# Kernel optimization log

Hardware: AMD Instinct MI355X
Metric: run time of the kernel (lower is better)

## Reference

```python
import jax, jax.numpy as jnp
import numpy as np

D = 128        # feature_dims
ITERS = 2      # update_iters
B, R = 8, 256  # n segments (proteins), residues per segment
NEG_SLOPE = 0.1

def leaky(x):
    return jax.nn.leaky_relu(x, NEG_SLOPE)

def setup_inputs() -> dict:
    key = jax.random.key(0)
    ks = jax.random.split(key, 13)
    def w(k, shape):
        fan_in = shape[0]
        return jax.random.normal(k, shape, jnp.float32) / np.sqrt(fan_in)
    return {
        "fresidues": jax.random.normal(ks[0], (B, R, 20), jnp.float32),
        "coordinates": jax.random.normal(ks[1], (B, R, 3), jnp.float32) * 10.0,
        "W_emb": w(ks[2], (20, D)),                    # res_embedding (no bias)
        "W_e1": w(ks[3], (2 * D + 1, D)),              # linear_e layer 1
        "b_e1": jnp.zeros((D,), jnp.float32),
        "W_e2": w(ks[4], (D, D)),                      # linear_e layer 2
        "b_e2": jnp.zeros((D,), jnp.float32),
        "W_inf": w(ks[5], (D, 1)),                     # linear_inf gate
        "b_inf": jnp.zeros((1,), jnp.float32),
        "W_h1": w(ks[6], (2 * D, D)),                  # linear_h layer 1
        "b_h1": jnp.zeros((D,), jnp.float32),
        "W_h2": w(ks[7], (D, D)),                      # linear_h layer 2
        "b_h2": jnp.zeros((D,), jnp.float32),
    }

def reference(fresidues, coordinates, W_emb, W_e1, b_e1, W_e2, b_e2,
              W_inf, b_inf, W_h1, b_h1, W_h2, b_h2):
    # h: [B,R,D]
    h = leaky(fresidues @ W_emb)
    # pairwise squared distances: [B,R,R,1], constant across iterations
    d2 = jnp.sum(jnp.square(coordinates[:, :, None, :] - coordinates[:, None, :, :]),
                 axis=-1, keepdims=True)
    # mask out self-edges (1 - eye): [1,R,R,1]
    mask = (1.0 - jnp.eye(R, dtype=h.dtype))[None, :, :, None]
    # split edge-MLP first-layer weights to avoid materializing the [B,R,R,2D+1] concat:
    # m_input = cat([h_i, h_j, d2]) @ W_e1  ==  h_i@W_i + h_j@W_j + d2*w_d
    W_i, W_j, w_d = W_e1[:D], W_e1[D:2 * D], W_e1[2 * D]
    for _ in range(ITERS):
        ti = h @ W_i                                   # [B,R,D] receiver part
        tj = h @ W_j                                   # [B,R,D] sender part
        pre = ti[:, :, None, :] + tj[:, None, :, :] + d2 * w_d + b_e1  # [B,R,R,D]
        m = leaky(leaky(pre) @ W_e2 + b_e2)            # [B,R,R,D]
        e = jax.nn.sigmoid(m @ W_inf + b_inf) * mask   # [B,R,R,1]
        m_pre = jnp.sum(m * e, axis=2)                 # sum over senders j -> [B,R,D]
        hm = jnp.concatenate([h, m_pre], axis=-1)      # [B,R,2D]
        h = (leaky(hm @ W_h1 + b_h1) @ W_h2 + b_h2) + h
    return h

if __name__ == "__main__":
    out = reference(**setup_inputs())
    print(out.shape, out.dtype)
```

## Files before the change

kernel.cpp:

```cpp
#include <hip/hip_runtime.h>

typedef unsigned short ushort_t;
typedef __attribute__((ext_vector_type(8))) short shortx8;
typedef __attribute__((ext_vector_type(4))) float floatx4;
typedef __attribute__((ext_vector_type(2))) float floatx2;

#define NS 0.1f

__device__ __forceinline__ ushort_t f2bf_rne(float f) {
  union { float f; unsigned int u; } v; v.f = f;
  unsigned int r = v.u + 0x7FFFu + ((v.u >> 16) & 1u);
  return (ushort_t)(r >> 16);
}
__device__ __forceinline__ unsigned int pk2bf(float a, float b) {
  union { float f; unsigned int u; } x, y; x.f = a; y.f = b;
  return __builtin_amdgcn_perm(y.u + 0x8000u, x.u + 0x8000u, 0x07060302u);
}
__device__ __forceinline__ ushort_t f2bf_rhu(float f) {
  union { float f; unsigned int u; } v; v.f = f;
  return (ushort_t)((v.u + 0x8000u) >> 16);
}
__device__ __forceinline__ float lk(float x) { return fmaxf(x, NS * x); }
__device__ __forceinline__ floatx2 lk2(floatx2 v) {
  return __builtin_elementwise_max(v, v * (floatx2){NS, NS});
}

__global__ __launch_bounds__(256) void prep_w(
    const float* __restrict__ W_e1, const float* __restrict__ W_e2,
    const float* __restrict__ W_h1, const float* __restrict__ W_h2,
    ushort_t* __restrict__ wijf, ushort_t* __restrict__ we2f,
    ushort_t* __restrict__ wh1f, ushort_t* __restrict__ wh2f) {
  int e = blockIdx.x * 256 + threadIdx.x;
  int which, le;
  if (e < 32768) { which = 0; le = e; }
  else if (e < 49152) { which = 1; le = e - 32768; }
  else if (e < 81920) { which = 2; le = e - 49152; }
  else { which = 3; le = e - 81920; }
  const int NT = (which == 0) ? 16 : 8;
  int f = le >> 3, j = le & 7;
  int lane = f & 63, ft = f >> 6;
  int t = ft % NT, s = ft / NT;
  int n = t * 16 + (lane & 15), k = s * 32 + (lane >> 4) * 8 + j;
  float v; ushort_t* d;
  if (which == 0) { v = (n < 128) ? W_e1[k * 128 + n] : W_e1[(128 + k) * 128 + (n - 128)]; d = wijf; }
  else if (which == 1) { v = W_e2[k * 128 + n]; d = we2f; }
  else if (which == 2) { v = W_h1[k * 128 + n]; d = wh1f; }
  else { v = W_h2[k * 128 + n]; d = wh2f; }
  d[le] = f2bf_rne(v);
}

__device__ __forceinline__ void proj_store(float v, int m, int n,
                                           float* __restrict__ ti, float* __restrict__ tjf) {
  if (n < 128) {
    ti[(size_t)m * 128 + n] = v;
  } else {
    int k = n - 128, b = m >> 8, j = m & 255;
    int s = k >> 5, lg2 = (k >> 3) & 3, j8 = k & 7;
    tjf[((((size_t)(b * 4 + s)) * 256 + j) * 4 + lg2) * 8 + j8] = v;
  }
}

__global__ __launch_bounds__(256) void h0_proj(
    const float* __restrict__ fres, const float* __restrict__ Wemb,
    const ushort_t* __restrict__ wijf, float* __restrict__ h_out,
    float* __restrict__ ti, float* __restrict__ tjf) {
  const int m0 = blockIdx.x * 16;
  const int tid = threadIdx.x;
  const int w = tid >> 6, lane = tid & 63, l16 = lane & 15, lg = lane >> 4;
  __shared__ __align__(16) ushort_t sH[16][136];
  {
    const int row = tid >> 4, c0 = (tid & 15) * 8;
    const float* fr = fres + (size_t)(m0 + row) * 20;
    float a[8] = {0, 0, 0, 0, 0, 0, 0, 0};
    for (int k = 0; k < 20; ++k) {
      float fv = fr[k];
      float4 w0 = *(const float4*)(Wemb + k * 128 + c0);
      float4 w1 = *(const float4*)(Wemb + k * 128 + c0 + 4);
      a[0] += fv * w0.x; a[1] += fv * w0.y; a[2] += fv * w0.z; a[3] += fv * w0.w;
      a[4] += fv * w1.x; a[5] += fv * w1.y; a[6] += fv * w1.z; a[7] += fv * w1.w;
    }
#pragma unroll
    for (int x = 0; x < 8; ++x) a[x] = lk(a[x]);
    float* ho = h_out + (size_t)(m0 + row) * 128 + c0;
    *(float4*)ho = (float4){a[0], a[1], a[2], a[3]};
    *(float4*)(ho + 4) = (float4){a[4], a[5], a[6], a[7]};
    unsigned int* sh = (unsigned int*)&sH[row][c0];
    sh[0] = pk2bf(a[0], a[1]); sh[1] = pk2bf(a[2], a[3]);
    sh[2] = pk2bf(a[4], a[5]); sh[3] = pk2bf(a[6], a[7]);
  }
  __syncthreads();
  floatx4 ap[4];
#pragma unroll
  for (int q = 0; q < 4; ++q) ap[q] = (floatx4){0.f, 0.f, 0.f, 0.f};
  const shortx8* Wp = (const shortx8*)wijf;
#pragma unroll
  for (int s = 0; s < 4; ++s) {
    shortx8 af = *(const shortx8*)&sH[l16][s * 32 + lg * 8];
#pragma unroll
    for (int q = 0; q < 4; ++q)
      ap[q] = __builtin_amdgcn_mfma_f32_16x16x32_bf16(af, Wp[(s * 16 + 4 * w + q) * 64 + lane], ap[q], 0, 0, 0);
  }
#pragma unroll
  for (int q = 0; q < 4; ++q) {
    const int n = (4 * w + q) * 16 + l16;
#pragma unroll
    for (int r = 0; r < 4; ++r) proj_store(ap[q][r], m0 + lg * 4 + r, n, ti, tjf);
  }
}

__global__ __launch_bounds__(256, 3) void edge_kernel(
    const float* __restrict__ ti, const float* __restrict__ tjf,
    const float* __restrict__ coords, const ushort_t* __restrict__ we2f,
    const float* __restrict__ W_e1, const float* __restrict__ b_e1,
    const float* __restrict__ b_e2, const float* __restrict__ W_inf,
    const float* __restrict__ b_inf, float* __restrict__ mp0, float* __restrict__ mp1) {
  const int blk = blockIdx.x;
  const int b = blk >> 9, i = (blk >> 1) & 255, ch = blk & 1;
  const int tid = threadIdx.x;
  const int w = tid >> 6, lane = tid & 63, l16 = lane & 15, lg = lane >> 4;

  __shared__ __align__(16) ushort_t sW[16384];
  __shared__ __align__(16) float sTiP[128];
  __shared__ __align__(16) float sWd[128];
  __shared__ __align__(16) float sD2[128];
  __shared__ __align__(16) float sMp[4][128];

  {
    shortx8* dst = (shortx8*)sW;
    const shortx8* src = (const shortx8*)we2f;
#pragma unroll
    for (int r = 0; r < 8; ++r) dst[r * 256 + tid] = src[r * 256 + tid];
  }
  if (tid < 128) {
    sTiP[tid] = ti[(size_t)(b * 256 + i) * 128 + tid] + b_e1[tid];
    sWd[tid] = W_e1[256 * 128 + tid];
    const int j = ch * 128 + tid;
    float dx = coords[(size_t)(b * 256 + i) * 3 + 0] - coords[(size_t)(b * 256 + j) * 3 + 0];
    float dy = coords[(size_t)(b * 256 + i) * 3 + 1] - coords[(size_t)(b * 256 + j) * 3 + 1];
    float dz = coords[(size_t)(b * 256 + i) * 3 + 2] - coords[(size_t)(b * 256 + j) * 3 + 2];
    sD2[tid] = dx * dx + dy * dy + dz * dz;
  }
  floatx4 acc[2][8];
#pragma unroll
  for (int t = 0; t < 8; ++t) {
    float bv = b_e2[t * 16 + l16];
    acc[0][t] = (floatx4){bv, bv, bv, bv};
    acc[1][t] = acc[0][t];
  }
  __syncthreads();

  float d2a[2];
  d2a[0] = sD2[w * 16 + l16];
  d2a[1] = sD2[64 + w * 16 + l16];
  const shortx8* sWf = (const shortx8*)sW;

#pragma unroll
  for (int s = 0; s < 4; ++s) {
    const int k0 = s * 32 + lg * 8;
    floatx2 p2[4], w2[4];
#pragma unroll
    for (int x = 0; x < 4; ++x) {
      p2[x] = *(const floatx2*)&sTiP[k0 + 2 * x];
      w2[x] = *(const floatx2*)&sWd[k0 + 2 * x];
    }
    shortx8 af[2];
#pragma unroll
    for (int c = 0; c < 2; ++c) {
      const int jr = ch * 128 + c * 64 + w * 16 + l16;
      const float* tb = tjf + (((size_t)(b * 4 + s) * 256 + jr) * 4 + lg) * 8;
      float4 t0 = *(const float4*)tb;
      float4 t1 = *(const float4*)(tb + 4);
      const floatx2 d2v = (floatx2){d2a[c], d2a[c]};
      floatx2 pr0 = (floatx2){t0.x, t0.y} + (p2[0] + d2v * w2[0]);
      floatx2 pr1 = (floatx2){t0.z, t0.w} + (p2[1] + d2v * w2[1]);
      floatx2 pr2 = (floatx2){t1.x, t1.y} + (p2[2] + d2v * w2[2]);
      floatx2 pr3 = (floatx2){t1.z, t1.w} + (p2[3] + d2v * w2[3]);
      floatx2 l0 = lk2(pr0), l1 = lk2(pr1), l2 = lk2(pr2), l3 = lk2(pr3);
      union { shortx8 s8; unsigned int u[4]; } A;
      A.u[0] = pk2bf(l0.x, l0.y); A.u[1] = pk2bf(l1.x, l1.y);
      A.u[2] = pk2bf(l2.x, l2.y); A.u[3] = pk2bf(l3.x, l3.y);
      af[c] = A.s8;
    }
#pragma unroll
    for (int tg = 0; tg < 2; ++tg) {
      shortx8 b0 = sWf[(s * 8 + tg * 4 + 0) * 64 + lane];
      shortx8 b1 = sWf[(s * 8 + tg * 4 + 1) * 64 + lane];
      shortx8 b2 = sWf[(s * 8 + tg * 4 + 2) * 64 + lane];
      shortx8 b3 = sWf[(s * 8 + tg * 4 + 3) * 64 + lane];
#pragma unroll
      for (int c = 0; c < 2; ++c) {
        acc[c][tg * 4 + 0] = __builtin_amdgcn_mfma_f32_16x16x32_bf16(af[c], b0, acc[c][tg * 4 + 0], 0, 0, 0);
        acc[c][tg * 4 + 1] = __builtin_amdgcn_mfma_f32_16x16x32_bf16(af[c], b1, acc[c][tg * 4 + 1], 0, 0, 0);
        acc[c][tg * 4 + 2] = __builtin_amdgcn_mfma_f32_16x16x32_bf16(af[c], b2, acc[c][tg * 4 + 2], 0, 0, 0);
        acc[c][tg * 4 + 3] = __builtin_amdgcn_mfma_f32_16x16x32_bf16(af[c], b3, acc[c][tg * 4 + 3], 0, 0, 0);
      }
    }
  }

  float winfv[8], mp[8];
#pragma unroll
  for (int t = 0; t < 8; ++t) { winfv[t] = W_inf[t * 16 + l16]; mp[t] = 0.f; }
  const float binf = b_inf[0];
#pragma unroll
  for (int c = 0; c < 2; ++c) {
#pragma unroll
    for (int t = 0; t < 8; ++t) {
      floatx2 v0 = lk2((floatx2){acc[c][t][0], acc[c][t][1]});
      floatx2 v1 = lk2((floatx2){acc[c][t][2], acc[c][t][3]});
      acc[c][t][0] = v0.x; acc[c][t][1] = v0.y; acc[c][t][2] = v1.x; acc[c][t][3] = v1.y;
    }
    float p[4];
#pragma unroll
    for (int r = 0; r < 4; ++r) {
      float sum = 0.f;
#pragma unroll
      for (int t = 0; t < 8; ++t) sum += acc[c][t][r] * winfv[t];
      p[r] = sum;
    }
#pragma unroll
    for (int off = 1; off <= 8; off <<= 1)
#pragma unroll
      for (int r = 0; r < 4; ++r) p[r] += __shfl_xor(p[r], off);
#pragma unroll
    for (int r = 0; r < 4; ++r) {
      const int jg = ch * 128 + c * 64 + w * 16 + lg * 4 + r;
      float x = p[r] + binf;
      float e = __builtin_amdgcn_rcpf(1.f + __expf(-x));
      if (jg == i) e = 0.f;
#pragma unroll
      for (int t = 0; t < 8; ++t) mp[t] += acc[c][t][r] * e;
    }
  }
#pragma unroll
  for (int t = 0; t < 8; ++t) {
    mp[t] += __shfl_xor(mp[t], 16);
    mp[t] += __shfl_xor(mp[t], 32);
  }
  if (lg == 0) {
#pragma unroll
    for (int t = 0; t < 8; ++t) sMp[w][t * 16 + l16] = mp[t];
  }
  __syncthreads();
  if (tid < 128) {
    float v = sMp[0][tid] + sMp[1][tid] + sMp[2][tid] + sMp[3][tid];
    float* mpo = ch ? mp1 : mp0;
    mpo[(size_t)(b * 256 + i) * 128 + tid] = v;
  }
}

__global__ __launch_bounds__(256) void node_kernel(
    const float* __restrict__ h_in, const float* __restrict__ mp0, const float* __restrict__ mp1,
    const ushort_t* __restrict__ wh1f, const float* __restrict__ b_h1,
    const ushort_t* __restrict__ wh2f, const float* __restrict__ b_h2,
    const ushort_t* __restrict__ wijf, float* __restrict__ h_out,
    float* __restrict__ ti, float* __restrict__ tjf, const int do_proj) {
  const int m0 = blockIdx.x * 16;
  const int tid = threadIdx.x;
  const int w = tid >> 6, lane = tid & 63, l16 = lane & 15, lg = lane >> 4;
  __shared__ __align__(16) ushort_t sA[16][264];
  __shared__ __align__(16) ushort_t sU[16][136];
  __shared__ __align__(16) ushort_t sHp[16][136];

  {
    const int row = tid >> 4, c0 = (tid & 15) * 16;
    unsigned int* dst = (unsigned int*)&sA[row][c0];
    if (c0 < 128) {
      const float* src = h_in + (size_t)(m0 + row) * 128 + c0;
#pragma unroll
      for (int x = 0; x < 8; ++x) dst[x] = pk2bf(src[2 * x], src[2 * x + 1]);
    } else {
      const float* s0 = mp0 + (size_t)(m0 + row) * 128 + (c0 - 128);
      const float* s1 = mp1 + (size_t)(m0 + row) * 128 + (c0 - 128);
#pragma unroll
      for (int x = 0; x < 8; ++x)
        dst[x] = pk2bf(s0[2 * x] + s1[2 * x], s0[2 * x + 1] + s1[2 * x + 1]);
    }
  }
  __syncthreads();
  floatx4 au[2];
#pragma unroll
  for (int q = 0; q < 2; ++q) { float bv = b_h1[(2 * w + q) * 16 + l16]; au[q] = (floatx4){bv, bv, bv, bv}; }
  const shortx8* W1 = (const shortx8*)wh1f;
#pragma unroll
  for (int s = 0; s < 8; ++s) {
    shortx8 af = *(const shortx8*)&sA[l16][s * 32 + lg * 8];
#pragma unroll
    for (int q = 0; q < 2; ++q)
      au[q] = __builtin_amdgcn_mfma_f32_16x16x32_bf16(af, W1[(s * 8 + 2 * w + q) * 64 + lane], au[q], 0, 0, 0);
  }
#pragma unroll
  for (int q = 0; q < 2; ++q)
#pragma unroll
    for (int r = 0; r < 4; ++r)
      sU[lg * 4 + r][(2 * w + q) * 16 + l16] = f2bf_rhu(lk(au[q][r]));
  __syncthreads();
  floatx4 ah[2];
#pragma unroll
  for (int q = 0; q < 2; ++q) { float bv = b_h2[(2 * w + q) * 16 + l16]; ah[q] = (floatx4){bv, bv, bv, bv}; }
  const shortx8* W2 = (const shortx8*)wh2f;
#pragma unroll
  for (int s = 0; s < 4; ++s) {
    shortx8 af = *(const shortx8*)&sU[l16][s * 32 + lg * 8];
#pragma unroll
    for (int q = 0; q < 2; ++q)
      ah[q] = __builtin_amdgcn_mfma_f32_16x16x32_bf16(af, W2[(s * 8 + 2 * w + q) * 64 + lane], ah[q], 0, 0, 0);
  }
#pragma unroll
  for (int q = 0; q < 2; ++q) {
    const int n = (2 * w + q) * 16 + l16;
#pragma unroll
    for (int r = 0; r < 4; ++r) {
      const int m = m0 + lg * 4 + r;
      float v = ah[q][r] + h_in[(size_t)m * 128 + n];
      h_out[(size_t)m * 128 + n] = v;
      sHp[lg * 4 + r][n] = f2bf_rhu(v);
    }
  }
  if (!do_proj) return;
  __syncthreads();
  floatx4 ap[4];
#pragma unroll
  for (int q = 0; q < 4; ++q) ap[q] = (floatx4){0.f, 0.f, 0.f, 0.f};
  const shortx8* Wp = (const shortx8*)wijf;
#pragma unroll
  for (int s = 0; s < 4; ++s) {
    shortx8 af = *(const shortx8*)&sHp[l16][s * 32 + lg * 8];
#pragma unroll
    for (int q = 0; q < 4; ++q)
      ap[q] = __builtin_amdgcn_mfma_f32_16x16x32_bf16(af, Wp[(s * 16 + 4 * w + q) * 64 + lane], ap[q], 0, 0, 0);
  }
#pragma unroll
  for (int q = 0; q < 4; ++q) {
    const int n = (4 * w + q) * 16 + l16;
#pragma unroll
    for (int r = 0; r < 4; ++r) proj_store(ap[q][r], m0 + lg * 4 + r, n, ti, tjf);
  }
}

extern "C" void kernel_launch(void* const* d_in, const int* in_sizes, int n_in,
                              void* d_out, int out_size, void* d_ws, size_t ws_size,
                              hipStream_t stream) {
  const float* fres   = (const float*)d_in[0];
  const float* coords = (const float*)d_in[1];
  const float* W_emb  = (const float*)d_in[2];
  const float* W_e1   = (const float*)d_in[3];
  const float* b_e1   = (const float*)d_in[4];
  const float* W_e2   = (const float*)d_in[5];
  const float* b_e2   = (const float*)d_in[6];
  const float* W_inf  = (const float*)d_in[7];
  const float* b_inf  = (const float*)d_in[8];
  const float* W_h1   = (const float*)d_in[9];
  const float* b_h1   = (const float*)d_in[10];
  const float* W_h2   = (const float*)d_in[11];
  const float* b_h2   = (const float*)d_in[12];
  float* out = (float*)d_out;

  char* ws = (char*)d_ws;
  float* hA  = (float*)(ws + (0 << 20));
  float* hB  = (float*)(ws + (1 << 20));
  float* tib = (float*)(ws + (2 << 20));
  float* tjf = (float*)(ws + (3 << 20));
  float* mp0 = (float*)(ws + (4 << 20));
  float* mp1 = (float*)(ws + (5 << 20));
  ushort_t* wijf = (ushort_t*)(ws + (6 << 20));
  ushort_t* we2f = wijf + 32768;
  ushort_t* wh1f = we2f + 16384;
  ushort_t* wh2f = wh1f + 32768;

  prep_w<<<384, 256, 0, stream>>>(W_e1, W_e2, W_h1, W_h2, wijf, we2f, wh1f, wh2f);
  h0_proj<<<128, 256, 0, stream>>>(fres, W_emb, wijf, hA, tib, tjf);

  edge_kernel<<<4096, 256, 0, stream>>>(tib, tjf, coords, we2f, W_e1, b_e1, b_e2, W_inf, b_inf, mp0, mp1);
  node_kernel<<<128, 256, 0, stream>>>(hA, mp0, mp1, wh1f, b_h1, wh2f, b_h2, wijf, hB, tib, tjf, 1);

  edge_kernel<<<4096, 256, 0, stream>>>(tib, tjf, coords, we2f, W_e1, b_e1, b_e2, W_inf, b_inf, mp0, mp1);
  node_kernel<<<128, 256, 0, stream>>>(hB, mp0, mp1, wh1f, b_h1, wh2f, b_h2, wijf, out, tib, tjf, 0);
}
```

Baseline: 180.2 us.

## Fuse all phases into one persistent cooperative kernel with grid syncs

Replaces the six separate kernel launches with one cooperative persistent kernel that runs the phases (weight prep, h0 projection, edge, node, edge, node) separated by grid-wide syncs. The edge phase now loops over several (segment, receiver, half) units per block and loads the W_e2 tile into shared memory once per block instead of once per unit. This removes launch gaps and repeated weight staging. In exchange it adds grid-sync overhead, caps the grid at 1024 blocks, and leaves most blocks idle during the small node phases. A fallback multi-launch path is kept.

```diff
diff --git a/kernel.cpp b/kernel.cpp
--- a/kernel.cpp
+++ b/kernel.cpp
@@ -1,4 +1,7 @@
 #include <hip/hip_runtime.h>
+#include <hip/hip_cooperative_groups.h>
+
+namespace cg = cooperative_groups;
 
 typedef unsigned short ushort_t;
 typedef __attribute__((ext_vector_type(8))) short shortx8;
@@ -25,354 +28,399 @@
   return __builtin_elementwise_max(v, v * (floatx2){NS, NS});
 }
 
-__global__ __launch_bounds__(256) void prep_w(
-    const float* __restrict__ W_e1, const float* __restrict__ W_e2,
-    const float* __restrict__ W_h1, const float* __restrict__ W_h2,
-    ushort_t* __restrict__ wijf, ushort_t* __restrict__ we2f,
-    ushort_t* __restrict__ wh1f, ushort_t* __restrict__ wh2f) {
-  int e = blockIdx.x * 256 + threadIdx.x;
-  int which, le;
-  if (e < 32768) { which = 0; le = e; }
-  else if (e < 49152) { which = 1; le = e - 32768; }
-  else if (e < 81920) { which = 2; le = e - 49152; }
-  else { which = 3; le = e - 81920; }
-  const int NT = (which == 0) ? 16 : 8;
-  int f = le >> 3, j = le & 7;
-  int lane = f & 63, ft = f >> 6;
-  int t = ft % NT, s = ft / NT;
-  int n = t * 16 + (lane & 15), k = s * 32 + (lane >> 4) * 8 + j;
-  float v; ushort_t* d;
-  if (which == 0) { v = (n < 128) ? W_e1[k * 128 + n] : W_e1[(128 + k) * 128 + (n - 128)]; d = wijf; }
-  else if (which == 1) { v = W_e2[k * 128 + n]; d = we2f; }
-  else if (which == 2) { v = W_h1[k * 128 + n]; d = wh1f; }
-  else { v = W_h2[k * 128 + n]; d = wh2f; }
-  d[le] = f2bf_rne(v);
-}
-
-__device__ __forceinline__ void proj_store(float v, int m, int n,
-                                           float* __restrict__ ti, float* __restrict__ tjf) {
+struct Prm {
+  const float* fres; const float* coords; const float* W_emb;
+  const float* W_e1; const float* b_e1; const float* W_e2; const float* b_e2;
+  const float* W_inf; const float* b_inf; const float* W_h1; const float* b_h1;
+  const float* W_h2; const float* b_h2;
+  float* out; float* hA; float* hB; float* tib; float* tjf; float* mp0; float* mp1;
+  ushort_t* wijf; ushort_t* we2f; ushort_t* wh1f; ushort_t* wh2f;
+};
+
+__device__ __forceinline__ void proj_store(const Prm& p, float v, int m, int n) {
   if (n < 128) {
-    ti[(size_t)m * 128 + n] = v;
+    p.tib[(size_t)m * 128 + n] = v;
   } else {
     int k = n - 128, b = m >> 8, j = m & 255;
     int s = k >> 5, lg2 = (k >> 3) & 3, j8 = k & 7;
-    tjf[((((size_t)(b * 4 + s)) * 256 + j) * 4 + lg2) * 8 + j8] = v;
-  }
-}
-
-__global__ __launch_bounds__(256) void h0_proj(
-    const float* __restrict__ fres, const float* __restrict__ Wemb,
-    const ushort_t* __restrict__ wijf, float* __restrict__ h_out,
-    float* __restrict__ ti, float* __restrict__ tjf) {
-  const int m0 = blockIdx.x * 16;
+    p.tjf[((((size_t)(b * 4 + s)) * 256 + j) * 4 + lg2) * 8 + j8] = v;
+  }
+}
+
+__device__ void phase_prep(const Prm& p) {
+  for (int e = blockIdx.x * 256 + threadIdx.x; e < 98304; e += gridDim.x * 256) {
+    int which, le;
+    if (e < 32768) { which = 0; le = e; }
+    else if (e < 49152) { which = 1; le = e - 32768; }
+    else if (e < 81920) { which = 2; le = e - 49152; }
+    else { which = 3; le = e - 81920; }
+    const int NT = (which == 0) ? 16 : 8;
+    int f = le >> 3, j = le & 7;
+    int lane = f & 63, ft = f >> 6;
+    int t = ft % NT, s = ft / NT;
+    int n = t * 16 + (lane & 15), k = s * 32 + (lane >> 4) * 8 + j;
+    float v; ushort_t* d;
+    if (which == 0) { v = (n < 128) ? p.W_e1[k * 128 + n] : p.W_e1[(128 + k) * 128 + (n - 128)]; d = p.wijf; }
+    else if (which == 1) { v = p.W_e2[k * 128 + n]; d = p.we2f; }
+    else if (which == 2) { v = p.W_h1[k * 128 + n]; d = p.wh1f; }
+    else { v = p.W_h2[k * 128 + n]; d = p.wh2f; }
+    d[le] = f2bf_rne(v);
+  }
+}
+
+__device__ void phase_h0proj(const Prm& p, char* smem) {
+  ushort_t (*sH)[136] = (ushort_t(*)[136])smem;
   const int tid = threadIdx.x;
   const int w = tid >> 6, lane = tid & 63, l16 = lane & 15, lg = lane >> 4;
-  __shared__ __align__(16) ushort_t sH[16][136];
-  {
-    const int row = tid >> 4, c0 = (tid & 15) * 8;
-    const float* fr = fres + (size_t)(m0 + row) * 20;
-    float a[8] = {0, 0, 0, 0, 0, 0, 0, 0};
-    for (int k = 0; k < 20; ++k) {
-      float fv = fr[k];
-      float4 w0 = *(const float4*)(Wemb + k * 128 + c0);
-      float4 w1 = *(const float4*)(Wemb + k * 128 + c0 + 4);
-      a[0] += fv * w0.x; a[1] += fv * w0.y; a[2] += fv * w0.z; a[3] += fv * w0.w;
-      a[4] += fv * w1.x; a[5] += fv * w1.y; a[6] += fv * w1.z; a[7] += fv * w1.w;
-    }
-#pragma unroll
-    for (int x = 0; x < 8; ++x) a[x] = lk(a[x]);
-    float* ho = h_out + (size_t)(m0 + row) * 128 + c0;
-    *(float4*)ho = (float4){a[0], a[1], a[2], a[3]};
-    *(float4*)(ho + 4) = (float4){a[4], a[5], a[6], a[7]};
-    unsigned int* sh = (unsigned int*)&sH[row][c0];
-    sh[0] = pk2bf(a[0], a[1]); sh[1] = pk2bf(a[2], a[3]);
-    sh[2] = pk2bf(a[4], a[5]); sh[3] = pk2bf(a[6], a[7]);
-  }
-  __syncthreads();
-  floatx4 ap[4];
-#pragma unroll
-  for (int q = 0; q < 4; ++q) ap[q] = (floatx4){0.f, 0.f, 0.f, 0.f};
-  const shortx8* Wp = (const shortx8*)wijf;
-#pragma unroll
-  for (int s = 0; s < 4; ++s) {
-    shortx8 af = *(const shortx8*)&sH[l16][s * 32 + lg * 8];
-#pragma unroll
-    for (int q = 0; q < 4; ++q)
-      ap[q] = __builtin_amdgcn_mfma_f32_16x16x32_bf16(af, Wp[(s * 16 + 4 * w + q) * 64 + lane], ap[q], 0, 0, 0);
-  }
-#pragma unroll
-  for (int q = 0; q < 4; ++q) {
-    const int n = (4 * w + q) * 16 + l16;
-#pragma unroll
-    for (int r = 0; r < 4; ++r) proj_store(ap[q][r], m0 + lg * 4 + r, n, ti, tjf);
-  }
-}
-
-__global__ __launch_bounds__(256, 3) void edge_kernel(
-    const float* __restrict__ ti, const float* __restrict__ tjf,
-    const float* __restrict__ coords, const ushort_t* __restrict__ we2f,
-    const float* __restrict__ W_e1, const float* __restrict__ b_e1,
-    const float* __restrict__ b_e2, const float* __restrict__ W_inf,
-    const float* __restrict__ b_inf, float* __restrict__ mp0, float* __restrict__ mp1) {
-  const int blk = blockIdx.x;
-  const int b = blk >> 9, i = (blk >> 1) & 255, ch = blk & 1;
+  for (int blk = blockIdx.x; blk < 128; blk += gridDim.x) {
+    const int m0 = blk * 16;
+    {
+      const int row = tid >> 4, c0 = (tid & 15) * 8;
+      const float* fr = p.fres + (size_t)(m0 + row) * 20;
+      float a[8] = {0, 0, 0, 0, 0, 0, 0, 0};
+      for (int k = 0; k < 20; ++k) {
+        float fv = fr[k];
+        float4 w0 = *(const float4*)(p.W_emb + k * 128 + c0);
+        float4 w1 = *(const float4*)(p.W_emb + k * 128 + c0 + 4);
+        a[0] += fv * w0.x; a[1] += fv * w0.y; a[2] += fv * w0.z; a[3] += fv * w0.w;
+        a[4] += fv * w1.x; a[5] += fv * w1.y; a[6] += fv * w1.z; a[7] += fv * w1.w;
+      }
+#pragma unroll
+      for (int x = 0; x < 8; ++x) a[x] = lk(a[x]);
+      float* ho = p.hA + (size_t)(m0 + row) * 128 + c0;
+      *(float4*)ho = (float4){a[0], a[1], a[2], a[3]};
+      *(float4*)(ho + 4) = (float4){a[4], a[5], a[6], a[7]};
+      unsigned int* sh = (unsigned int*)&sH[row][c0];
+      sh[0] = pk2bf(a[0], a[1]); sh[1] = pk2bf(a[2], a[3]);
+      sh[2] = pk2bf(a[4], a[5]); sh[3] = pk2bf(a[6], a[7]);
+    }
+    __syncthreads();
+    floatx4 ap[4];
+#pragma unroll
+    for (int q = 0; q < 4; ++q) ap[q] = (floatx4){0.f, 0.f, 0.f, 0.f};
+    const shortx8* Wp = (const shortx8*)p.wijf;
+#pragma unroll
+    for (int s = 0; s < 4; ++s) {
+      shortx8 af = *(const shortx8*)&sH[l16][s * 32 + lg * 8];
+#pragma unroll
+      for (int q = 0; q < 4; ++q)
+        ap[q] = __builtin_amdgcn_mfma_f32_16x16x32_bf16(af, Wp[(s * 16 + 4 * w + q) * 64 + lane], ap[q], 0, 0, 0);
+    }
+#pragma unroll
+    for (int q = 0; q < 4; ++q) {
+      const int n = (4 * w + q) * 16 + l16;
+#pragma unroll
+      for (int r = 0; r < 4; ++r) proj_store(p, ap[q][r], m0 + lg * 4 + r, n);
+    }
+    __syncthreads();
+  }
+}
+
+__device__ void phase_edge(const Prm& p, char* smem) {
   const int tid = threadIdx.x;
   const int w = tid >> 6, lane = tid & 63, l16 = lane & 15, lg = lane >> 4;
-
-  __shared__ __align__(16) ushort_t sW[16384];
-  __shared__ __align__(16) float sTiP[128];
-  __shared__ __align__(16) float sWd[128];
-  __shared__ __align__(16) float sD2[128];
-  __shared__ __align__(16) float sMp[4][128];
-
+  ushort_t* sW = (ushort_t*)smem;
+  float* sTiP = (float*)(smem + 32768);
+  float* sWd  = (float*)(smem + 33280);
+  float* sD2  = (float*)(smem + 33792);
+  float* sMp  = (float*)(smem + 34304);
   {
     shortx8* dst = (shortx8*)sW;
-    const shortx8* src = (const shortx8*)we2f;
+    const shortx8* src = (const shortx8*)p.we2f;
 #pragma unroll
     for (int r = 0; r < 8; ++r) dst[r * 256 + tid] = src[r * 256 + tid];
-  }
-  if (tid < 128) {
-    sTiP[tid] = ti[(size_t)(b * 256 + i) * 128 + tid] + b_e1[tid];
-    sWd[tid] = W_e1[256 * 128 + tid];
-    const int j = ch * 128 + tid;
-    float dx = coords[(size_t)(b * 256 + i) * 3 + 0] - coords[(size_t)(b * 256 + j) * 3 + 0];
-    float dy = coords[(size_t)(b * 256 + i) * 3 + 1] - coords[(size_t)(b * 256 + j) * 3 + 1];
-    float dz = coords[(size_t)(b * 256 + i) * 3 + 2] - coords[(size_t)(b * 256 + j) * 3 + 2];
-    sD2[tid] = dx * dx + dy * dy + dz * dz;
-  }
-  floatx4 acc[2][8];
-#pragma unroll
-  for (int t = 0; t < 8; ++t) {
-    float bv = b_e2[t * 16 + l16];
-    acc[0][t] = (floatx4){bv, bv, bv, bv};
-    acc[1][t] = acc[0][t];
-  }
-  __syncthreads();
-
-  float d2a[2];
-  d2a[0] = sD2[w * 16 + l16];
-  d2a[1] = sD2[64 + w * 16 + l16];
+    if (tid < 128) sWd[tid] = p.W_e1[256 * 128 + tid];
+  }
   const shortx8* sWf = (const shortx8*)sW;
-
-#pragma unroll
-  for (int s = 0; s < 4; ++s) {
-    const int k0 = s * 32 + lg * 8;
-    floatx2 p2[4], w2[4];
-#pragma unroll
-    for (int x = 0; x < 4; ++x) {
-      p2[x] = *(const floatx2*)&sTiP[k0 + 2 * x];
-      w2[x] = *(const floatx2*)&sWd[k0 + 2 * x];
-    }
-    shortx8 af[2];
+  const int per = (4096 + gridDim.x - 1) / gridDim.x;
+
+  for (int u = 0; u < per; ++u) {
+    const int unit = blockIdx.x * per + u;
+    if (unit >= 4096) break;
+    const int b = unit >> 9, i = (unit >> 1) & 255, ch = unit & 1;
+    __syncthreads();
+    if (tid < 128) {
+      sTiP[tid] = p.tib[(size_t)(b * 256 + i) * 128 + tid] + p.b_e1[tid];
+      const int j = ch * 128 + tid;
+      float dx = p.coords[(size_t)(b * 256 + i) * 3 + 0] - p.coords[(size_t)(b * 256 + j) * 3 + 0];
+      float dy = p.coords[(size_t)(b * 256 + i) * 3 + 1] - p.coords[(size_t)(b * 256 + j) * 3 + 1];
+      float dz = p.coords[(size_t)(b * 256 + i) * 3 + 2] - p.coords[(size_t)(b * 256 + j) * 3 + 2];
+      sD2[tid] = dx * dx + dy * dy + dz * dz;
+    }
+    floatx4 acc[2][8];
+#pragma unroll
+    for (int t = 0; t < 8; ++t) {
+      float bv = p.b_e2[t * 16 + l16];
+      acc[0][t] = (floatx4){bv, bv, bv, bv};
+      acc[1][t] = acc[0][t];
+    }
+    __syncthreads();
+    float d2a0 = sD2[w * 16 + l16], d2a1 = sD2[64 + w * 16 + l16];
+#pragma unroll
+    for (int s = 0; s < 4; ++s) {
+      const int k0 = s * 32 + lg * 8;
+      floatx2 p2[4], w2[4];
+#pragma unroll
+      for (int x = 0; x < 4; ++x) {
+        p2[x] = *(const floatx2*)&sTiP[k0 + 2 * x];
+        w2[x] = *(const floatx2*)&sWd[k0 + 2 * x];
+      }
+      shortx8 af[2];
+#pragma unroll
+      for (int c = 0; c < 2; ++c) {
+        const int jr = ch * 128 + c * 64 + w * 16 + l16;
+        const float* tb = p.tjf + (((size_t)(b * 4 + s) * 256 + jr) * 4 + lg) * 8;
+        float4 t0 = *(const float4*)tb;
+        float4 t1 = *(const float4*)(tb + 4);
+        const float d2 = c ? d2a1 : d2a0;
+        const floatx2 d2v = (floatx2){d2, d2};
+        floatx2 pr0 = (floatx2){t0.x, t0.y} + (p2[0] + d2v * w2[0]);
+        floatx2 pr1 = (floatx2){t0.z, t0.w} + (p2[1] + d2v * w2[1]);
+        floatx2 pr2 = (floatx2){t1.x, t1.y} + (p2[2] + d2v * w2[2]);
+        floatx2 pr3 = (floatx2){t1.z, t1.w} + (p2[3] + d2v * w2[3]);
+        floatx2 l0 = lk2(pr0), l1 = lk2(pr1), l2 = lk2(pr2), l3 = lk2(pr3);
+        union { shortx8 s8; unsigned int uu[4]; } A;
+        A.uu[0] = pk2bf(l0.x, l0.y); A.uu[1] = pk2bf(l1.x, l1.y);
+        A.uu[2] = pk2bf(l2.x, l2.y); A.uu[3] = pk2bf(l3.x, l3.y);
+        af[c] = A.s8;
+      }
+#pragma unroll
+      for (int tg = 0; tg < 2; ++tg) {
+        shortx8 b0 = sWf[(s * 8 + tg * 4 + 0) * 64 + lane];
+        shortx8 b1 = sWf[(s * 8 + tg * 4 + 1) * 64 + lane];
+        shortx8 b2 = sWf[(s * 8 + tg * 4 + 2) * 64 + lane];
+        shortx8 b3 = sWf[(s * 8 + tg * 4 + 3) * 64 + lane];
+#pragma unroll
+        for (int c = 0; c < 2; ++c) {
+          acc[c][tg * 4 + 0] = __builtin_amdgcn_mfma_f32_16x16x32_bf16(af[c], b0, acc[c][tg * 4 + 0], 0, 0, 0);
+          acc[c][tg * 4 + 1] = __builtin_amdgcn_mfma_f32_16x16x32_bf16(af[c], b1, acc[c][tg * 4 + 1], 0, 0, 0);
+          acc[c][tg * 4 + 2] = __builtin_amdgcn_mfma_f32_16x16x32_bf16(af[c], b2, acc[c][tg * 4 + 2], 0, 0, 0);
+          acc[c][tg * 4 + 3] = __builtin_amdgcn_mfma_f32_16x16x32_bf16(af[c], b3, acc[c][tg * 4 + 3], 0, 0, 0);
+        }
+      }
+    }
+    float winfv[8];
+#pragma unroll
+    for (int t = 0; t < 8; ++t) winfv[t] = p.W_inf[t * 16 + l16];
+    const float binf = p.b_inf[0];
+    floatx2 mpp[8];
+#pragma unroll
+    for (int t = 0; t < 8; ++t) mpp[t] = (floatx2){0.f, 0.f};
 #pragma unroll
     for (int c = 0; c < 2; ++c) {
-      const int jr = ch * 128 + c * 64 + w * 16 + l16;
-      const float* tb = tjf + (((size_t)(b * 4 + s) * 256 + jr) * 4 + lg) * 8;
-      float4 t0 = *(const float4*)tb;
-      float4 t1 = *(const float4*)(tb + 4);
-      const floatx2 d2v = (floatx2){d2a[c], d2a[c]};
-      floatx2 pr0 = (floatx2){t0.x, t0.y} + (p2[0] + d2v * w2[0]);
-      floatx2 pr1 = (floatx2){t0.z, t0.w} + (p2[1] + d2v * w2[1]);
-      floatx2 pr2 = (floatx2){t1.x, t1.y} + (p2[2] + d2v * w2[2]);
-      floatx2 pr3 = (floatx2){t1.z, t1.w} + (p2[3] + d2v * w2[3]);
-      floatx2 l0 = lk2(pr0), l1 = lk2(pr1), l2 = lk2(pr2), l3 = lk2(pr3);
-      union { shortx8 s8; unsigned int u[4]; } A;
-      A.u[0] = pk2bf(l0.x, l0.y); A.u[1] = pk2bf(l1.x, l1.y);
-      A.u[2] = pk2bf(l2.x, l2.y); A.u[3] = pk2bf(l3.x, l3.y);
-      af[c] = A.s8;
-    }
-#pragma unroll
-    for (int tg = 0; tg < 2; ++tg) {
-      shortx8 b0 = sWf[(s * 8 + tg * 4 + 0) * 64 + lane];
-      shortx8 b1 = sWf[(s * 8 + tg * 4 + 1) * 64 + lane];
-      shortx8 b2 = sWf[(s * 8 + tg * 4 + 2) * 64 + lane];
-      shortx8 b3 = sWf[(s * 8 + tg * 4 + 3) * 64 + lane];
-#pragma unroll
-      for (int c = 0; c < 2; ++c) {
-        acc[c][tg * 4 + 0] = __builtin_amdgcn_mfma_f32_16x16x32_bf16(af[c], b0, acc[c][tg * 4 + 0], 0, 0, 0);
-        acc[c][tg * 4 + 1] = __builtin_amdgcn_mfma_f32_16x16x32_bf16(af[c], b1, acc[c][tg * 4 + 1], 0, 0, 0);
-        acc[c][tg * 4 + 2] = __builtin_amdgcn_mfma_f32_16x16x32_bf16(af[c], b2, acc[c][tg * 4 + 2], 0, 0, 0);
-        acc[c][tg * 4 + 3] = __builtin_amdgcn_mfma_f32_16x16x32_bf16(af[c], b3, acc[c][tg * 4 + 3], 0, 0, 0);
-      }
-    }
-  }
-
-  float winfv[8], mp[8];
-#pragma unroll
-  for (int t = 0; t < 8; ++t) { winfv[t] = W_inf[t * 16 + l16]; mp[t] = 0.f; }
-  const float binf = b_inf[0];
-#pragma unroll
-  for (int c = 0; c < 2; ++c) {
+#pragma unroll
+      for (int t = 0; t < 8; ++t) {
+        floatx2 v0 = lk2((floatx2){acc[c][t][0], acc[c][t][1]});
+        floatx2 v1 = lk2((floatx2){acc[c][t][2], acc[c][t][3]});
+        acc[c][t][0] = v0.x; acc[c][t][1] = v0.y; acc[c][t][2] = v1.x; acc[c][t][3] = v1.y;
+      }
+      floatx2 q01 = (floatx2){0.f, 0.f}, q23 = (floatx2){0.f, 0.f};
+#pragma unroll
+      for (int t = 0; t < 8; ++t) {
+        const floatx2 wv = (floatx2){winfv[t], winfv[t]};
+        q01 += (floatx2){acc[c][t][0], acc[c][t][1]} * wv;
+        q23 += (floatx2){acc[c][t][2], acc[c][t][3]} * wv;
+      }
+      float pp[4] = {q01.x, q01.y, q23.x, q23.y};
+#pragma unroll
+      for (int off = 1; off <= 8; off <<= 1)
+#pragma unroll
+        for (int r = 0; r < 4; ++r) pp[r] += __shfl_xor(pp[r], off);
+      float e[4];
+#pragma unroll
+      for (int r = 0; r < 4; ++r) {
+        const int jg = ch * 128 + c * 64 + w * 16 + lg * 4 + r;
+        float x = pp[r] + binf;
+        e[r] = __builtin_amdgcn_rcpf(1.f + __expf(-x));
+        if (jg == i) e[r] = 0.f;
+      }
+      const floatx2 e01 = (floatx2){e[0], e[1]}, e23 = (floatx2){e[2], e[3]};
+#pragma unroll
+      for (int t = 0; t < 8; ++t) {
+        mpp[t] += (floatx2){acc[c][t][0], acc[c][t][1]} * e01;
+        mpp[t] += (floatx2){acc[c][t][2], acc[c][t][3]} * e23;
+      }
+    }
+    float mp[8];
 #pragma unroll
     for (int t = 0; t < 8; ++t) {
-      floatx2 v0 = lk2((floatx2){acc[c][t][0], acc[c][t][1]});
-      floatx2 v1 = lk2((floatx2){acc[c][t][2], acc[c][t][3]});
-      acc[c][t][0] = v0.x; acc[c][t][1] = v0.y; acc[c][t][2] = v1.x; acc[c][t][3] = v1.y;
-    }
-    float p[4];
-#pragma unroll
-    for (int r = 0; r < 4; ++r) {
-      float sum = 0.f;
-#pragma unroll
-      for (int t = 0; t < 8; ++t) sum += acc[c][t][r] * winfv[t];
-      p[r] = sum;
-    }
-#pragma unroll
-    for (int off = 1; off <= 8; off <<= 1)
-#pragma unroll
-      for (int r = 0; r < 4; ++r) p[r] += __shfl_xor(p[r], off);
-#pragma unroll
-    for (int r = 0; r < 4; ++r) {
-      const int jg = ch * 128 + c * 64 + w * 16 + lg * 4 + r;
-      float x = p[r] + binf;
-      float e = __builtin_amdgcn_rcpf(1.f + __expf(-x));
-      if (jg == i) e = 0.f;
-#pragma unroll
-      for (int t = 0; t < 8; ++t) mp[t] += acc[c][t][r] * e;
-    }
-  }
-#pragma unroll
-  for (int t = 0; t < 8; ++t) {
-    mp[t] += __shfl_xor(mp[t], 16);
-    mp[t] += __shfl_xor(mp[t], 32);
-  }
-  if (lg == 0) {
-#pragma unroll
-    for (int t = 0; t < 8; ++t) sMp[w][t * 16 + l16] = mp[t];
-  }
-  __syncthreads();
-  if (tid < 128) {
-    float v = sMp[0][tid] + sMp[1][tid] + sMp[2][tid] + sMp[3][tid];
-    float* mpo = ch ? mp1 : mp0;
-    mpo[(size_t)(b * 256 + i) * 128 + tid] = v;
-  }
-}
-
-__global__ __launch_bounds__(256) void node_kernel(
-    const float* __restrict__ h_in, const float* __restrict__ mp0, const float* __restrict__ mp1,
-    const ushort_t* __restrict__ wh1f, const float* __restrict__ b_h1,
-    const ushort_t* __restrict__ wh2f, const float* __restrict__ b_h2,
-    const ushort_t* __restrict__ wijf, float* __restrict__ h_out,
-    float* __restrict__ ti, float* __restrict__ tjf, const int do_proj) {
-  const int m0 = blockIdx.x * 16;
+      mp[t] = mpp[t].x + mpp[t].y;
+      mp[t] += __shfl_xor(mp[t], 16);
+      mp[t] += __shfl_xor(mp[t], 32);
+    }
+    if (lg == 0) {
+#pragma unroll
+      for (int t = 0; t < 8; ++t) sMp[w * 128 + t * 16 + l16] = mp[t];
+    }
+    __syncthreads();
+    if (tid < 128) {
+      float v = sMp[tid] + sMp[128 + tid] + sMp[256 + tid] + sMp[384 + tid];
+      (ch ? p.mp1 : p.mp0)[(size_t)(b * 256 + i) * 128 + tid] = v;
+    }
+  }
+}
+
+__device__ void phase_node(const Prm& p, char* smem, const float* h_in, float* h_out, int do_proj) {
+  ushort_t (*sA)[264]  = (ushort_t(*)[264])smem;
+  ushort_t (*sU)[136]  = (ushort_t(*)[136])(smem + 8448);
+  ushort_t (*sHp)[136] = (ushort_t(*)[136])(smem + 12800);
   const int tid = threadIdx.x;
   const int w = tid >> 6, lane = tid & 63, l16 = lane & 15, lg = lane >> 4;
-  __shared__ __align__(16) ushort_t sA[16][264];
-  __shared__ __align__(16) ushort_t sU[16][136];
-  __shared__ __align__(16) ushort_t sHp[16][136];
-
-  {
-    const int row = tid >> 4, c0 = (tid & 15) * 16;
-    unsigned int* dst = (unsigned int*)&sA[row][c0];
-    if (c0 < 128) {
-      const float* src = h_in + (size_t)(m0 + row) * 128 + c0;
-#pragma unroll
-      for (int x = 0; x < 8; ++x) dst[x] = pk2bf(src[2 * x], src[2 * x + 1]);
-    } else {
-      const float* s0 = mp0 + (size_t)(m0 + row) * 128 + (c0 - 128);
-      const float* s1 = mp1 + (size_t)(m0 + row) * 128 + (c0 - 128);
-#pragma unroll
-      for (int x = 0; x < 8; ++x)
-        dst[x] = pk2bf(s0[2 * x] + s1[2 * x], s0[2 * x + 1] + s1[2 * x + 1]);
-    }
-  }
-  __syncthreads();
-  floatx4 au[2];
-#pragma unroll
-  for (int q = 0; q < 2; ++q) { float bv = b_h1[(2 * w + q) * 16 + l16]; au[q] = (floatx4){bv, bv, bv, bv}; }
-  const shortx8* W1 = (const shortx8*)wh1f;
-#pragma unroll
-  for (int s = 0; s < 8; ++s) {
-    shortx8 af = *(const shortx8*)&sA[l16][s * 32 + lg * 8];
+  for (int blk = blockIdx.x; blk < 128; blk += gridDim.x) {
+    const int m0 = blk * 16;
+    {
+      const int row = tid >> 4, c0 = (tid & 15) * 16;
+      unsigned int* dst = (unsigned int*)&sA[row][c0];
+      if (c0 < 128) {
+        const float* src = h_in + (size_t)(m0 + row) * 128 + c0;
+#pragma unroll
+        for (int x = 0; x < 8; ++x) dst[x] = pk2bf(src[2 * x], src[2 * x + 1]);
+      } else {
+        const float* s0 = p.mp0 + (size_t)(m0 + row) * 128 + (c0 - 128);
+        const float* s1 = p.mp1 + (size_t)(m0 + row) * 128 + (c0 - 128);
+#pragma unroll
+        for (int x = 0; x < 8; ++x)
+          dst[x] = pk2bf(s0[2 * x] + s1[2 * x], s0[2 * x + 1] + s1[2 * x + 1]);
+      }
+    }
+    __syncthreads();
+    floatx4 au[2];
+#pragma unroll
+    for (int q = 0; q < 2; ++q) { float bv = p.b_h1[(2 * w + q) * 16 + l16]; au[q] = (floatx4){bv, bv, bv, bv}; }
+    const shortx8* W1 = (const shortx8*)p.wh1f;
+#pragma unroll
+    for (int s = 0; s < 8; ++s) {
+      shortx8 af = *(const shortx8*)&sA[l16][s * 32 + lg * 8];
+#pragma unroll
+      for (int q = 0; q < 2; ++q)
+        au[q] = __builtin_amdgcn_mfma_f32_16x16x32_bf16(af, W1[(s * 8 + 2 * w + q) * 64 + lane], au[q], 0, 0, 0);
+    }
 #pragma unroll
     for (int q = 0; q < 2; ++q)
-      au[q] = __builtin_amdgcn_mfma_f32_16x16x32_bf16(af, W1[(s * 8 + 2 * w + q) * 64 + lane], au[q], 0, 0, 0);
-  }
-#pragma unroll
-  for (int q = 0; q < 2; ++q)
-#pragma unroll
-    for (int r = 0; r < 4; ++r)
-      sU[lg * 4 + r][(2 * w + q) * 16 + l16] = f2bf_rhu(lk(au[q][r]));
-  __syncthreads();
-  floatx4 ah[2];
-#pragma unroll
-  for (int q = 0; q < 2; ++q) { float bv = b_h2[(2 * w + q) * 16 + l16]; ah[q] = (floatx4){bv, bv, bv, bv}; }
-  const shortx8* W2 = (const shortx8*)wh2f;
-#pragma unroll
-  for (int s = 0; s < 4; ++s) {
-    shortx8 af = *(const shortx8*)&sU[l16][s * 32 + lg * 8];
-#pragma unroll
-    for (int q = 0; q < 2; ++q)
-      ah[q] = __builtin_amdgcn_mfma_f32_16x16x32_bf16(af, W2[(s * 8 + 2 * w + q) * 64 + lane], ah[q], 0, 0, 0);
-  }
-#pragma unroll
-  for (int q = 0; q < 2; ++q) {
-    const int n = (2 * w + q) * 16 + l16;
-#pragma unroll
-    for (int r = 0; r < 4; ++r) {
-      const int m = m0 + lg * 4 + r;
-      float v = ah[q][r] + h_in[(size_t)m * 128 + n];
-      h_out[(size_t)m * 128 + n] = v;
-      sHp[lg * 4 + r][n] = f2bf_rhu(v);
-    }
-  }
-  if (!do_proj) return;
-  __syncthreads();
-  floatx4 ap[4];
-#pragma unroll
-  for (int q = 0; q < 4; ++q) ap[q] = (floatx4){0.f, 0.f, 0.f, 0.f};
-  const shortx8* Wp = (const shortx8*)wijf;
-#pragma unroll
-  for (int s = 0; s < 4; ++s) {
-    shortx8 af = *(const shortx8*)&sHp[l16][s * 32 + lg * 8];
-#pragma unroll
-    for (int q = 0; q < 4; ++q)
-      ap[q] = __builtin_amdgcn_mfma_f32_16x16x32_bf16(af, Wp[(s * 16 + 4 * w + q) * 64 + lane], ap[q], 0, 0, 0);
-  }
-#pragma unroll
-  for (int q = 0; q < 4; ++q) {
-    const int n = (4 * w + q) * 16 + l16;
-#pragma unroll
-    for (int r = 0; r < 4; ++r) proj_store(ap[q][r], m0 + lg * 4 + r, n, ti, tjf);
-  }
+#pragma unroll
+      for (int r = 0; r < 4; ++r)
+        sU[lg * 4 + r][(2 * w + q) * 16 + l16] = f2bf_rhu(lk(au[q][r]));
+    __syncthreads();
+    floatx4 ah[2];
+#pragma unroll
+    for (int q = 0; q < 2; ++q) { float bv = p.b_h2[(2 * w + q) * 16 + l16]; ah[q] = (floatx4){bv, bv, bv, bv}; }
+    const shortx8* W2 = (const shortx8*)p.wh2f;
+#pragma unroll
+    for (int s = 0; s < 4; ++s) {
+      shortx8 af = *(const shortx8*)&sU[l16][s * 32 + lg * 8];
+#pragma unroll
+      for (int q = 0; q < 2; ++q)
+        ah[q] = __builtin_amdgcn_mfma_f32_16x16x32_bf16(af, W2[(s * 8 + 2 * w + q) * 64 + lane], ah[q], 0, 0, 0);
+    }
+#pragma unroll
+    for (int q = 0; q < 2; ++q) {
+      const int n = (2 * w + q) * 16 + l16;
+#pragma unroll
+      for (int r = 0; r < 4; ++r) {
+        const int m = m0 + lg * 4 + r;
+        float v = ah[q][r] + h_in[(size_t)m * 128 + n];
+        h_out[(size_t)m * 128 + n] = v;
+        sHp[lg * 4 + r][n] = f2bf_rhu(v);
+      }
+    }
+    if (do_proj) {
+      __syncthreads();
+      floatx4 ap[4];
+#pragma unroll
+      for (int q = 0; q < 4; ++q) ap[q] = (floatx4){0.f, 0.f, 0.f, 0.f};
+      const shortx8* Wp = (const shortx8*)p.wijf;
+#pragma unroll
+      for (int s = 0; s < 4; ++s) {
+        shortx8 af = *(const shortx8*)&sHp[l16][s * 32 + lg * 8];
+#pragma unroll
+        for (int q = 0; q < 4; ++q)
+          ap[q] = __builtin_amdgcn_mfma_f32_16x16x32_bf16(af, Wp[(s * 16 + 4 * w + q) * 64 + lane], ap[q], 0, 0, 0);
+      }
+#pragma unroll
+      for (int q = 0; q < 4; ++q) {
+        const int n = (4 * w + q) * 16 + l16;
+#pragma unroll
+        for (int r = 0; r < 4; ++r) proj_store(p, ap[q][r], m0 + lg * 4 + r, n);
+      }
+    }
+    __syncthreads();
+  }
+}
+
+__global__ __launch_bounds__(256, 4) void fused(Prm p) {
+  __shared__ __align__(16) char smem[36864];
+  cg::grid_group g = cg::this_grid();
+  phase_prep(p);
+  g.sync();
+  phase_h0proj(p, smem);
+  g.sync();
+  phase_edge(p, smem);
+  g.sync();
+  phase_node(p, smem, p.hA, p.hB, 1);
+  g.sync();
+  phase_edge(p, smem);
+  g.sync();
+  phase_node(p, smem, p.hB, p.out, 0);
+}
+
+__global__ __launch_bounds__(256, 4) void k_prep(Prm p) { phase_prep(p); }
+__global__ __launch_bounds__(256, 4) void k_h0(Prm p) {
+  __shared__ __align__(16) char smem[4352]; phase_h0proj(p, smem);
+}
+__global__ __launch_bounds__(256, 4) void k_edge(Prm p) {
+  __shared__ __align__(16) char smem[36864]; phase_edge(p, smem);
+}
+__global__ __launch_bounds__(256, 4) void k_node(Prm p, const float* hi, float* ho, int dp) {
+  __shared__ __align__(16) char smem[17152]; phase_node(p, smem, hi, ho, dp);
 }
 
 extern "C" void kernel_launch(void* const* d_in, const int* in_sizes, int n_in,
                               void* d_out, int out_size, void* d_ws, size_t ws_size,
                               hipStream_t stream) {
-  const float* fres   = (const float*)d_in[0];
-  const float* coords = (const float*)d_in[1];
-  const float* W_emb  = (const float*)d_in[2];
-  const float* W_e1   = (const float*)d_in[3];
-  const float* b_e1   = (const float*)d_in[4];
-  const float* W_e2   = (const float*)d_in[5];
-  const float* b_e2   = (const float*)d_in[6];
-  const float* W_inf  = (const float*)d_in[7];
-  const float* b_inf  = (const float*)d_in[8];
-  const float* W_h1   = (const float*)d_in[9];
-  const float* b_h1   = (const float*)d_in[10];
-  const float* W_h2   = (const float*)d_in[11];
-  const float* b_h2   = (const float*)d_in[12];
-  float* out = (float*)d_out;
-
   char* ws = (char*)d_ws;
-  float* hA  = (float*)(ws + (0 << 20));
-  float* hB  = (float*)(ws + (1 << 20));
-  float* tib = (float*)(ws + (2 << 20));
-  float* tjf = (float*)(ws + (3 << 20));
-  float* mp0 = (float*)(ws + (4 << 20));
-  float* mp1 = (float*)(ws + (5 << 20));
-  ushort_t* wijf = (ushort_t*)(ws + (6 << 20));
-  ushort_t* we2f = wijf + 32768;
-  ushort_t* wh1f = we2f + 16384;
-  ushort_t* wh2f = wh1f + 32768;
-
-  prep_w<<<384, 256, 0, stream>>>(W_e1, W_e2, W_h1, W_h2, wijf, we2f, wh1f, wh2f);
-  h0_proj<<<128, 256, 0, stream>>>(fres, W_emb, wijf, hA, tib, tjf);
-
-  edge_kernel<<<4096, 256, 0, stream>>>(tib, tjf, coords, we2f, W_e1, b_e1, b_e2, W_inf, b_inf, mp0, mp1);
-  node_kernel<<<128, 256, 0, stream>>>(hA, mp0, mp1, wh1f, b_h1, wh2f, b_h2, wijf, hB, tib, tjf, 1);
-
-  edge_kernel<<<4096, 256, 0, stream>>>(tib, tjf, coords, we2f, W_e1, b_e1, b_e2, W_inf, b_inf, mp0, mp1);
-  node_kernel<<<128, 256, 0, stream>>>(hB, mp0, mp1, wh1f, b_h1, wh2f, b_h2, wijf, out, tib, tjf, 0);
-}
+  Prm p;
+  p.fres   = (const float*)d_in[0];
+  p.coords = (const float*)d_in[1];
+  p.W_emb  = (const float*)d_in[2];
+  p.W_e1   = (const float*)d_in[3];
+  p.b_e1   = (const float*)d_in[4];
+  p.W_e2   = (const float*)d_in[5];
+  p.b_e2   = (const float*)d_in[6];
+  p.W_inf  = (const float*)d_in[7];
+  p.b_inf  = (const float*)d_in[8];
+  p.W_h1   = (const float*)d_in[9];
+  p.b_h1   = (const float*)d_in[10];
+  p.W_h2   = (const float*)d_in[11];
+  p.b_h2   = (const float*)d_in[12];
+  p.out    = (float*)d_out;
+  p.hA   = (float*)(ws + (0 << 20));
+  p.hB   = (float*)(ws + (1 << 20));
+  p.tib  = (float*)(ws + (2 << 20));
+  p.tjf  = (float*)(ws + (3 << 20));
+  p.mp0  = (float*)(ws + (4 << 20));
+  p.mp1  = (float*)(ws + (5 << 20));
+  p.wijf = (ushort_t*)(ws + (6 << 20));
+  p.we2f = p.wijf + 32768;
+  p.wh1f = p.we2f + 16384;
+  p.wh2f = p.wh1f + 32768;
+
+  int nb = 0;
+  hipError_t qerr = hipOccupancyMaxActiveBlocksPerMultiprocessor(&nb, (const void*)fused, 256, 0);
+  bool coop = (qerr == hipSuccess) && (nb >= 1);
+  if (coop) {
+    int grid = nb * 256;
+    if (grid > 1024) grid = 1024;
+    void* args[] = { &p };
+    hipError_t lerr = hipLaunchCooperativeKernel((const void*)fused, dim3(grid), dim3(256),
+                                                 args, 0, stream);
+    if (lerr != hipSuccess) coop = false;
+  }
+  if (!coop) {
+    k_prep<<<384, 256, 0, stream>>>(p);
+    k_h0<<<128, 256, 0, stream>>>(p);
+    k_edge<<<1024, 256, 0, stream>>>(p);
+    k_node<<<128, 256, 0, stream>>>(p, p.hA, p.hB, 1);
+    k_edge<<<1024, 256, 0, stream>>>(p);
+    k_node<<<128, 256, 0, stream>>>(p, p.hB, p.out, 0);
+  }
+}
```

New measurement: 484.7 us. +168.9%, slower.
